# Kernel optimization log

Hardware: AMD Instinct MI355X
Metric: run time of the kernel (lower is better)

## Reference

```python
import jax, jax.numpy as jnp
import numpy as np

B, T, D, CHUNK = 8, 4096, 256, 64
ETA_SCALE = 1e-3
EPS = 1e-6


def setup_inputs() -> dict:
    key = jax.random.key(0)
    ks = jax.random.split(key, 16)
    s = 1.0 / np.sqrt(D)
    def w(k, shape):
        return jax.random.uniform(k, shape, jnp.float32, -s, s)
    return {
        'x': jax.random.normal(ks[0], (B, T, D), jnp.float32),
        'k_w1': w(ks[1], (D, D)), 'k_w2': w(ks[2], (D, D)),
        'v_w1': w(ks[3], (D, D)), 'v_w2': w(ks[4], (D, D)),
        'q_w1': w(ks[5], (D, D)), 'q_w2': w(ks[6], (D, D)),
        'eta_w1': w(ks[7], (1, D)), 'eta_w2': w(ks[8], (D, D)), 'eta_wskip': w(ks[9], (1, D)),
        'alpha_w1': w(ks[10], (1, D)), 'alpha_w2': w(ks[11], (D, D)), 'alpha_wskip': w(ks[12], (1, D)),
        'mem_w1': w(ks[13], (D, D)), 'mem_w2': w(ks[14], (D, D)),
    }


def _gelu(z):
    return jax.nn.gelu(z, approximate=False)  # torch F.gelu default = exact erf gelu


def _dgelu(z):
    # d/dz [z * Phi(z)] = Phi(z) + z * pdf(z)
    cdf = 0.5 * (1.0 + jax.lax.erf(z * (1.0 / np.sqrt(2.0))))
    pdf = jnp.exp(-0.5 * z * z) * (1.0 / np.sqrt(2.0 * np.pi))
    return cdf + z * pdf


def _mem_fwd(x, w1, w2, wskip):
    z = jnp.einsum('bti,bhi->bth', x, w2)
    h = _gelu(z)
    res = x if wskip is None else jnp.einsum('bti,boi->bto', x, wskip)
    return res + jnp.einsum('bth,boh->bto', h, w1)


def _l2norm(q):
    n = jnp.sqrt(jnp.sum(q * q, axis=-1, keepdims=True))
    return q / jnp.maximum(n, EPS)


def _update(st, k, v, eta, abar):
    # chunked DGD: theta <- (prod_t alpha_t) * theta - sum_t eta_t * grad ||M(k_t) - v_t||^2
    w1, w2, wskip = st
    z = jnp.einsum('bti,bhi->bth', k, w2)
    h = _gelu(z)
    res = k if wskip is None else jnp.einsum('bti,boi->bto', k, wskip)
    f = res + jnp.einsum('bth,boh->bto', h, w1)  # [b,t,out]
    if w1.shape[1] == v.shape[-1]:
        g = 2.0 * (f - v)
    else:  # out_dim==1 memories: broadcasted l2 -> reduce over broadcast dim
        g = 2.0 * jnp.sum(f - v, axis=-1, keepdims=True)
    gW1 = jnp.einsum('bto,bth,bt->boh', g, h, eta)
    pre = jnp.einsum('bto,boh->bth', g, w1) * _dgelu(z)
    gW2 = jnp.einsum('bth,bti,bt->bhi', pre, k, eta)
    a = abar[:, None, None]
    nskip = None if wskip is None else a * wskip - jnp.einsum('bto,bti,bt->boi', g, k, eta)
    return (a * w1 - gW1, a * w2 - gW2, nskip)


def _forward(x, k_w1, k_w2, v_w1, v_w2, q_w1, q_w2, eta_w1, eta_w2, eta_wskip,
             alpha_w1, alpha_w2, alpha_wskip, mem_w1, mem_w2):
    b, t, d = x.shape
    def bt(w):
        return jnp.broadcast_to(w[None], (b,) + w.shape)
    states = (
        (bt(k_w1), bt(k_w2), None),
        (bt(v_w1), bt(v_w2), None),
        (bt(q_w1), bt(q_w2), None),
        (bt(eta_w1), bt(eta_w2), bt(eta_wskip)),
        (bt(alpha_w1), bt(alpha_w2), bt(alpha_wskip)),
        (bt(mem_w1), bt(mem_w2), None),
    )
    nc = t // CHUNK
    xc = x.reshape(b, nc, CHUNK, d).transpose(1, 0, 2, 3)  # [NC, B, C, D]

    def step(states, xch):
        sk, sv, sq, se, sa, sm = states
        k = _l2norm(_mem_fwd(xch, *sk))
        v = _mem_fwd(xch, *sv)
        q = _l2norm(_mem_fwd(xch, *sq))
        eta = jax.nn.softplus(_mem_fwd(xch, *se)[..., 0]) * ETA_SCALE
        alpha = jax.nn.sigmoid(_mem_fwd(xch, *sa)[..., 0])
        o = _mem_fwd(q, *sm)
        abar = jnp.prod(alpha, axis=1)  # [b]
        new = tuple(_update(s, k, v, eta, abar) for s in (sk, sv, sq, se, sa, sm))
        return new, o

    _, ys = jax.lax.scan(step, states, xc)  # [NC, B, C, D]
    return ys.transpose(1, 0, 2, 3).reshape(b, t, d)


def reference(x, k_w1, k_w2, v_w1, v_w2, q_w1, q_w2, eta_w1, eta_w2, eta_wskip,
              alpha_w1, alpha_w2, alpha_wskip, mem_w1, mem_w2):
    return _forward(x, k_w1, k_w2, v_w1, v_w2, q_w1, q_w2, eta_w1, eta_w2, eta_wskip,
                    alpha_w1, alpha_w2, alpha_wskip, mem_w1, mem_w2)
```

## Files before the change

### kernel.cpp

```cpp
#include <hip/hip_runtime.h>
#include <hip/hip_bf16.h>
#include <math.h>

constexpr int NB  = 8;
constexpr int TT  = 4096;
constexpr int DD  = 256;
constexpr int CK  = 64;
constexpr int NCK = 64;
constexpr float ETA_SC = 1e-3f;
constexpr float EPSV   = 1e-6f;

constexpr size_t MSZ = (size_t)DD*DD;

constexpr size_t OFF_W2  = 0;
constexpr size_t OFF_W1B = OFF_W2  + (size_t)NB*6*MSZ;
constexpr size_t OFF_W1S = OFF_W1B + (size_t)NB*4*MSZ;
constexpr size_t OFF_WSK = OFF_W1S + (size_t)NB*2*DD;
constexpr size_t OFF_SCK = OFF_WSK + (size_t)NB*2*DD;
constexpr size_t OFF_SCQ = OFF_SCK + (size_t)NB*CK;
constexpr size_t OFF_VSUM= OFF_SCQ + (size_t)NB*CK;
constexpr size_t OFF_ETA = OFF_VSUM+ (size_t)NB*CK;
constexpr size_t OFF_GS  = OFF_ETA + (size_t)NB*CK;
constexpr size_t OFF_SALP= OFF_GS  + (size_t)NB*2*CK;
constexpr size_t OFF_ABAR= OFF_SALP+ (size_t)NB*CK;
constexpr size_t OFF_BARC= OFF_ABAR + NB;
constexpr size_t FTOT    = OFF_BARC + NB;

constexpr size_t BOFF_F  = 0;
constexpr size_t BOFF_H  = BOFF_F  + (size_t)3*NB*CK*DD;
constexpr size_t BOFF_GB = BOFF_H  + (size_t)NB*6*CK*DD;
constexpr size_t BOFF_P  = BOFF_GB + (size_t)NB*4*CK*DD;

__device__ __forceinline__ int bigIdx(int m){ return (m==5)?3:m; }

__device__ __forceinline__ float geluf(float z){
  return 0.5f*z*(1.0f + erff(z*0.70710678118654752440f));
}
__device__ __forceinline__ float dgeluf(float z){
  float cdf = 0.5f*(1.0f + erff(z*0.70710678118654752440f));
  float pdf = expf(-0.5f*z*z)*0.39894228040143267794f;
  return cdf + z*pdf;
}
__device__ __forceinline__ float bfu(unsigned short u){
  unsigned int v = ((unsigned int)u)<<16;
  return __uint_as_float(v);
}
__device__ __forceinline__ float wsum(float v){
  #pragma unroll
  for (int off=32; off>0; off>>=1) v += __shfl_xor(v, off, 64);
  return v;
}

__device__ __forceinline__ void bbar(unsigned int* cnt, unsigned int target){
  __syncthreads();
  if (threadIdx.x == 0){
    __threadfence();
    atomicAdd(cnt, 1u);
    unsigned int it = 0;
    while (__hip_atomic_load(cnt, __ATOMIC_RELAXED, __HIP_MEMORY_SCOPE_AGENT) < target
           && ++it < (1u<<18))
      __builtin_amdgcn_s_sleep(2);
    __threadfence();
  }
  __syncthreads();
}

__device__ __forceinline__ void gfull(const float* __restrict__ sA,
      const float* __restrict__ Wm, int cg, int rg, float acc[4][4]){
  #pragma unroll 4
  for (int kk=0; kk<256; kk+=4){
    float4 w0 = *(const float4*)(Wm + (size_t)(cg      )*DD + kk);
    float4 w1 = *(const float4*)(Wm + (size_t)(cg +  64)*DD + kk);
    float4 w2 = *(const float4*)(Wm + (size_t)(cg + 128)*DD + kk);
    float4 w3 = *(const float4*)(Wm + (size_t)(cg + 192)*DD + kk);
    #pragma unroll
    for (int rr=0; rr<4; rr++){
      float4 a = *(const float4*)(sA + (rg*4+rr)*260 + kk);
      acc[rr][0] += a.x*w0.x + a.y*w0.y + a.z*w0.z + a.w*w0.w;
      acc[rr][1] += a.x*w1.x + a.y*w1.y + a.z*w1.z + a.w*w1.w;
      acc[rr][2] += a.x*w2.x + a.y*w2.y + a.z*w2.z + a.w*w2.w;
      acc[rr][3] += a.x*w3.x + a.y*w3.y + a.z*w3.z + a.w*w3.w;
    }
  }
}

__device__ __forceinline__ void gfullT(const float* __restrict__ sA,
      const float* __restrict__ Wm, int cg, int rg, float acc[4][4]){
  #pragma unroll 2
  for (int kk=0; kk<256; kk+=4){
    float wv[4][4];
    #pragma unroll
    for (int s=0;s<4;s++)
      #pragma unroll
      for (int j=0;j<4;j++)
        wv[s][j] = Wm[(size_t)(kk+s)*DD + cg+64*j];
    #pragma unroll
    for (int rr=0;rr<4;rr++){
      float4 a = *(const float4*)(sA + (rg*4+rr)*260 + kk);
      #pragma unroll
      for (int j=0;j<4;j++)
        acc[rr][j] += a.x*wv[0][j] + a.y*wv[1][j] + a.z*wv[2][j] + a.w*wv[3][j];
    }
  }
}

__global__ __launch_bounds__(256) void initk(float* __restrict__ W,
  const float* kw1, const float* kw2, const float* vw1, const float* vw2,
  const float* qw1, const float* qw2, const float* ew1, const float* ew2,
  const float* ewsk, const float* aw1, const float* aw2, const float* awsk,
  const float* mw1, const float* mw2)
{
  int b = blockIdx.x/6, m = blockIdx.x%6;
  const float *w1s=nullptr,*w2s=nullptr,*wsks=nullptr;
  switch(m){
    case 0: w1s=kw1; w2s=kw2; break;
    case 1: w1s=vw1; w2s=vw2; break;
    case 2: w1s=qw1; w2s=qw2; break;
    case 3: w1s=ew1; w2s=ew2; wsks=ewsk; break;
    case 4: w1s=aw1; w2s=aw2; wsks=awsk; break;
    default: w1s=mw1; w2s=mw2; break;
  }
  if (m==0 && threadIdx.x==0)
    ((unsigned int*)(W + OFF_BARC))[b] = 0u;
  float* w2d = W + OFF_W2 + ((size_t)b*6+m)*MSZ;
  for (size_t i=threadIdx.x; i<MSZ; i+=256) w2d[i] = w2s[i];
  if (m==3 || m==4){
    int sm = m-3;
    float* w1d = W + OFF_W1S + ((size_t)b*2+sm)*DD;
    float* wsd = W + OFF_WSK + ((size_t)b*2+sm)*DD;
    for (int i=threadIdx.x;i<DD;i+=256){ w1d[i]=w1s[i]; wsd[i]=wsks[i]; }
  } else {
    float* w1d = W + OFF_W1B + ((size_t)b*4+bigIdx(m))*MSZ;
    for (size_t i=threadIdx.x;i<MSZ;i+=256) w1d[i] = w1s[i];
  }
}

__global__ __launch_bounds__(256, 1) void pers(const float* __restrict__ x,
        float* __restrict__ W, __hip_bfloat16* __restrict__ B,
        float* __restrict__ out)
{
  const int blk = blockIdx.x, tid = threadIdx.x;
  const int b = blk & 7, wb = blk >> 3;
  const int cg = tid & 63, rg = tid >> 6;
  unsigned int* cnt = ((unsigned int*)(W + OFF_BARC)) + b;
  unsigned int bar = 0;
  __shared__ __align__(16) float sMem[2*16*260];
  __shared__ float sSc[64];
  __shared__ float sEt[64], sSk[64];
  float* sX = sMem;
  float* sY = sMem + 16*260;

  for (int ck=0; ck<NCK; ck++){
    for (int task=wb; task<20; task+=32){
      int m = task>>2, t0 = (task&3)*16;
      const float* xp = x + ((size_t)b*TT + (size_t)ck*CK + t0)*DD;
      for (int l=tid; l<1024; l+=256){
        int tl = l>>6, ii = (l&63)<<2;
        *(float4*)(sX + tl*260 + ii) = *(const float4*)(xp + (size_t)tl*DD + ii);
      }
      __syncthreads();
      const float* w2 = W + OFF_W2 + ((size_t)b*6+m)*MSZ;
      float acc1[4][4];
      #pragma unroll
      for (int i=0;i<4;i++){ acc1[i][0]=acc1[i][1]=acc1[i][2]=acc1[i][3]=0.0f; }
      gfull(sX, w2, cg, rg, acc1);
      if (m < 3){
        #pragma unroll
        for (int rr=0;rr<4;rr++)
          #pragma unroll
          for (int j=0;j<4;j++)
            sY[(rg*4+rr)*260 + cg+64*j] = geluf(acc1[rr][j]);
        __syncthreads();
        const float* w1 = W + OFF_W1B + ((size_t)b*4+m)*MSZ;
        float acc2[4][4];
        #pragma unroll
        for (int i=0;i<4;i++){ acc2[i][0]=acc2[i][1]=acc2[i][2]=acc2[i][3]=0.0f; }
        gfull(sY, w1, cg, rg, acc2);
        __hip_bfloat16* fd = B + BOFF_F + ((size_t)m*NB + b)*CK*DD;
        float p[4];
        #pragma unroll
        for (int rr=0;rr<4;rr++){
          float ps = 0.0f;
          #pragma unroll
          for (int j=0;j<4;j++){
            int col = cg+64*j;
            float F = sX[(rg*4+rr)*260 + col] + acc2[rr][j];
            fd[(size_t)(t0+rg*4+rr)*DD + col] = __float2bfloat16(F);
            ps += (m==1) ? F : F*F;
          }
          p[rr] = ps;
        }
        #pragma unroll
        for (int rr=0;rr<4;rr++){
          float v = wsum(p[rr]);
          if (cg == 0){
            int t = t0 + rg*4 + rr;
            if (m==0)      W[OFF_SCK + (size_t)b*CK + t] = 1.0f/fmaxf(sqrtf(v), EPSV);
            else if (m==2) W[OFF_SCQ + (size_t)b*CK + t] = 1.0f/fmaxf(sqrtf(v), EPSV);
            else           W[OFF_VSUM+ (size_t)b*CK + t] = v;
          }
        }
      } else {
        int sm = m-3;
        const float* w1s = W + OFF_W1S + ((size_t)b*2+sm)*DD;
        const float* wsk = W + OFF_WSK + ((size_t)b*2+sm)*DD;
        float p[4];
        #pragma unroll
        for (int rr=0;rr<4;rr++){
          float ps = 0.0f;
          #pragma unroll
          for (int j=0;j<4;j++){
            int col = cg+64*j;
            ps += sX[(rg*4+rr)*260+col]*wsk[col] + geluf(acc1[rr][j])*w1s[col];
          }
          p[rr] = ps;
        }
        #pragma unroll
        for (int rr=0;rr<4;rr++){
          float v = wsum(p[rr]);
          if (cg == 0){
            int t = t0 + rg*4 + rr;
            if (sm==0){
              float sp = (v>0.0f) ? (v + log1pf(expf(-v))) : log1pf(expf(v));
              W[OFF_ETA + (size_t)b*CK + t] = sp*ETA_SC;
            } else {
              W[OFF_SALP + (size_t)b*CK + t] = 1.0f/(1.0f+expf(-v));
            }
          }
        }
      }
      __syncthreads();
    }
    bar += 32; bbar(cnt, bar);

    for (int task=wb; task<29; task+=32){
      if (task < 28){
        int chn = task>>2, t0 = (task&3)*16;
        bool isq = (chn==6);
        const unsigned short* fsrc = (const unsigned short*)
            (B + BOFF_F + ((size_t)(isq?2:0)*NB + b)*CK*DD + (size_t)t0*DD);
        const float* scp = W + (isq?OFF_SCQ:OFF_SCK) + (size_t)b*CK + t0;
        if (tid < 16)       sSc[tid] = scp[tid];
        else if (tid < 32)  sSc[tid] = W[OFF_ETA + (size_t)b*CK + t0 + (tid-16)];
        else if (tid < 48)  sSc[tid] = W[OFF_VSUM+ (size_t)b*CK + t0 + (tid-32)];
        __syncthreads();
        for (int l=tid; l<1024; l+=256){
          int tl = l>>6, ii = (l&63)<<2;
          ushort4 u = *(const ushort4*)(fsrc + (size_t)tl*DD + ii);
          float s = sSc[tl];
          float4 t4;
          t4.x = bfu(u.x)*s; t4.y = bfu(u.y)*s; t4.z = bfu(u.z)*s; t4.w = bfu(u.w)*s;
          *(float4*)(sX + tl*260 + ii) = t4;
        }
        __syncthreads();
        int m2 = isq ? 5 : chn;
        const float* w2 = W + OFF_W2 + ((size_t)b*6+m2)*MSZ;
        float acc1[4][4];
        #pragma unroll
        for (int i=0;i<4;i++){ acc1[i][0]=acc1[i][1]=acc1[i][2]=acc1[i][3]=0.0f; }
        gfull(sX, w2, cg, rg, acc1);

        if (chn==0 || chn==1 || chn==2 || chn==5){
          int mi = (chn==5)?3:chn;
          __hip_bfloat16* hd = B + BOFF_H + ((size_t)(b*6+chn))*CK*DD;
          #pragma unroll
          for (int rr=0;rr<4;rr++)
            #pragma unroll
            for (int j=0;j<4;j++){
              float h = geluf(acc1[rr][j]);
              sY[(rg*4+rr)*260 + cg+64*j] = h;
              hd[(size_t)(t0+rg*4+rr)*DD + cg+64*j] = __float2bfloat16(h);
            }
          __syncthreads();
          const float* w1 = W + OFF_W1B + ((size_t)b*4+mi)*MSZ;
          float acc2[4][4];
          #pragma unroll
          for (int i=0;i<4;i++){ acc2[i][0]=acc2[i][1]=acc2[i][2]=acc2[i][3]=0.0f; }
          gfull(sY, w1, cg, rg, acc2);
          __syncthreads();
          const unsigned short* fv = (const unsigned short*)
              (B + BOFF_F + ((size_t)1*NB + b)*CK*DD + (size_t)t0*DD);
          __hip_bfloat16* gd = B + BOFF_GB + ((size_t)(b*4+mi))*CK*DD;
          #pragma unroll
          for (int rr=0;rr<4;rr++)
            #pragma unroll
            for (int j=0;j<4;j++){
              int col = cg+64*j;
              float g = 2.0f*( sX[(rg*4+rr)*260+col] + acc2[rr][j]
                               - bfu(fv[(size_t)(rg*4+rr)*DD+col]) );
              sY[(rg*4+rr)*260+col] = g;
              gd[(size_t)(t0+rg*4+rr)*DD + col] = __float2bfloat16(g);
            }
          __syncthreads();
          float accp[4][4];
          #pragma unroll
          for (int i=0;i<4;i++){ accp[i][0]=accp[i][1]=accp[i][2]=accp[i][3]=0.0f; }
          gfullT(sY, w1, cg, rg, accp);
          __hip_bfloat16* pd2 = B + BOFF_P + ((size_t)(b*6+chn))*CK*DD;
          #pragma unroll
          for (int rr=0;rr<4;rr++){
            float et = sSc[16 + rg*4+rr];
            #pragma unroll
            for (int j=0;j<4;j++)
              pd2[(size_t)(t0+rg*4+rr)*DD + cg+64*j] =
                __float2bfloat16(accp[rr][j]*dgeluf(acc1[rr][j])*et);
          }
        } else if (chn==6){
          #pragma unroll
          for (int rr=0;rr<4;rr++)
            #pragma unroll
            for (int j=0;j<4;j++)
              sY[(rg*4+rr)*260 + cg+64*j] = geluf(acc1[rr][j]);
          __syncthreads();
          const float* w1 = W + OFF_W1B + ((size_t)b*4+3)*MSZ;
          float acc2[4][4];
          #pragma unroll
          for (int i=0;i<4;i++){ acc2[i][0]=acc2[i][1]=acc2[i][2]=acc2[i][3]=0.0f; }
          gfull(sY, w1, cg, rg, acc2);
          float* op = out + ((size_t)b*TT + (size_t)ck*CK + t0)*DD;
          #pragma unroll
          for (int rr=0;rr<4;rr++)
            #pragma unroll
            for (int j=0;j<4;j++){
              int col = cg+64*j;
              op[(size_t)(rg*4+rr)*DD + col] = sX[(rg*4+rr)*260+col] + acc2[rr][j];
            }
        } else {
          int sm = chn-3;
          __hip_bfloat16* hd = B + BOFF_H + ((size_t)(b*6+chn))*CK*DD;
          const float* w1s = W + OFF_W1S + ((size_t)b*2+sm)*DD;
          const float* wsk = W + OFF_WSK + ((size_t)b*2+sm)*DD;
          float p[4];
          #pragma unroll
          for (int rr=0;rr<4;rr++){
            float ps = 0.0f;
            #pragma unroll
            for (int j=0;j<4;j++){
              int col = cg+64*j;
              float h = geluf(acc1[rr][j]);
              hd[(size_t)(t0+rg*4+rr)*DD + col] = __float2bfloat16(h);
              ps += sX[(rg*4+rr)*260+col]*wsk[col] + h*w1s[col];
            }
            p[rr] = ps;
          }
          __hip_bfloat16* pd2 = B + BOFF_P + ((size_t)(b*6+chn))*CK*DD;
          #pragma unroll
          for (int rr=0;rr<4;rr++){
            float f = wsum(p[rr]);
            int t = t0 + rg*4 + rr;
            float gs = 2.0f*(256.0f*f - sSc[32 + rg*4+rr]);
            if (cg == 0) W[OFF_GS + ((size_t)b*2+sm)*CK + t] = gs;
            float ge = gs * sSc[16 + rg*4+rr];
            #pragma unroll
            for (int j=0;j<4;j++){
              int col = cg+64*j;
              pd2[(size_t)t*DD + col] =
                __float2bfloat16(ge*w1s[col]*dgeluf(acc1[rr][j]));
            }
          }
        }
      } else {
        if (tid < 64){
          float v = W[OFF_SALP + (size_t)b*CK + tid];
          #pragma unroll
          for (int off=32; off>0; off>>=1) v *= __shfl_xor(v, off, 64);
          if (tid == 0) W[OFF_ABAR + b] = v;
        }
      }
      __syncthreads();
    }
    bar += 32; bbar(cnt, bar);

    {
      if (tid < 64){
        sEt[tid] = W[OFF_ETA + (size_t)b*CK + tid];
        sSk[tid] = W[OFF_SCK + (size_t)b*CK + tid];
      }
      __syncthreads();
      float ab = W[OFF_ABAR + b];
      const unsigned short* fk = (const unsigned short*)(B + BOFF_F + ((size_t)0*NB+b)*CK*DD);
      float* sT = sMem;
      int c = tid;
      for (int task=wb; task<82; task+=32){
        if (task < 32){
          int mi = task>>3, o0 = (task&7)*32;
          int m = (mi==3)?5:mi;
          const unsigned short* hb = (const unsigned short*)(B + BOFF_H + ((size_t)(b*6+m))*CK*DD);
          const unsigned short* gb = (const unsigned short*)(B + BOFF_GB + ((size_t)(b*4+mi))*CK*DD);
          float* w1 = W + OFF_W1B + ((size_t)b*4+mi)*MSZ;
          float hv[64];
          #pragma unroll
          for (int t=0;t<64;t++) hv[t] = bfu(hb[(size_t)t*DD + c]);
          for (int l=tid; l<2048; l+=256){
            int t=l>>5, oo=l&31;
            sT[oo*68+t] = bfu(gb[(size_t)t*DD + o0+oo]) * sEt[t];
          }
          __syncthreads();
          for (int oo=0; oo<32; oo++){
            float s = 0.0f;
            #pragma unroll
            for (int t4=0; t4<16; t4++){
              float4 g4 = *(const float4*)(sT + oo*68 + t4*4);
              s += g4.x*hv[4*t4] + g4.y*hv[4*t4+1] + g4.z*hv[4*t4+2] + g4.w*hv[4*t4+3];
            }
            size_t idx = (size_t)(o0+oo)*DD + c;
            w1[idx] = ab*w1[idx] - s;
          }
        } else if (task < 80){
          int r = task-32, m = r>>3, h0 = (r&7)*32;
          const unsigned short* pd2 = (const unsigned short*)(B + BOFF_P + ((size_t)(b*6+m))*CK*DD);
          float* w2 = W + OFF_W2 + ((size_t)b*6+m)*MSZ;
          float kc[64];
          #pragma unroll
          for (int t=0;t<64;t++) kc[t] = bfu(fk[(size_t)t*DD+c]) * sSk[t];
          for (int l=tid; l<2048; l+=256){
            int t=l>>5, hh=l&31;
            sT[hh*68+t] = bfu(pd2[(size_t)t*DD + h0+hh]);
          }
          __syncthreads();
          for (int hh=0; hh<32; hh++){
            float s = 0.0f;
            #pragma unroll
            for (int t4=0; t4<16; t4++){
              float4 p4 = *(const float4*)(sT + hh*68 + t4*4);
              s += p4.x*kc[4*t4] + p4.y*kc[4*t4+1] + p4.z*kc[4*t4+2] + p4.w*kc[4*t4+3];
            }
            size_t idx = (size_t)(h0+hh)*DD + c;
            w2[idx] = ab*w2[idx] - s;
          }
        } else {
          int sm = task-80, m = 3+sm;
          const unsigned short* hb = (const unsigned short*)(B + BOFF_H + ((size_t)(b*6+m))*CK*DD);
          float s1=0.0f, s2=0.0f;
          #pragma unroll
          for (int t=0;t<64;t++){
            float ge = W[OFF_GS + ((size_t)b*2+sm)*CK + t] * sEt[t];
            s1 += ge * bfu(hb[(size_t)t*DD+c]);
            s2 += ge * bfu(fk[(size_t)t*DD+c]) * sSk[t];
          }
          float* w1s = W + OFF_W1S + ((size_t)b*2+sm)*DD;
          float* wskp= W + OFF_WSK + ((size_t)b*2+sm)*DD;
          w1s[c]  = ab*w1s[c]  - s1;
          wskp[c] = ab*wskp[c] - s2;
        }
        __syncthreads();
      }
    }
    bar += 32; bbar(cnt, bar);
  }
}

extern "C" void kernel_launch(void* const* d_in, const int* in_sizes, int n_in,
                              void* d_out, int out_size, void* d_ws, size_t ws_size,
                              hipStream_t stream){
  const float* x = (const float*)d_in[0];
  float* W = (float*)d_ws;
  __hip_bfloat16* B = (__hip_bfloat16*)(W + FTOT);
  float* out = (float*)d_out;

  initk<<<NB*6, 256, 0, stream>>>(W,
      (const float*)d_in[1], (const float*)d_in[2],
      (const float*)d_in[3], (const float*)d_in[4],
      (const float*)d_in[5], (const float*)d_in[6],
      (const float*)d_in[7], (const float*)d_in[8],
      (const float*)d_in[9], (const float*)d_in[10],
      (const float*)d_in[11], (const float*)d_in[12],
      (const float*)d_in[13], (const float*)d_in[14]);

  pers<<<256, 256, 0, stream>>>(x, W, B, out);
}
```

Baseline: 15.06 ms.

## Store weights transposed for coalesced GEMV loads and keep dual W1 copies

Weights are now stored transposed (W2T, W1T) so each thread reads contiguous float4 columns, which coalesces the global loads in the forward GEMMs. A second, untransposed W1 copy serves the backward product, replacing the strided gfullT path. Stores of h, g and p switch to vectorized ushort4 and float4, and the update phase is retiled into 64-wide tasks. The cost is updating two copies of W1 per chunk, extra memory, and fewer update tasks, so load balance across the 32 worker blocks changes.

```diff
diff --git a/kernel.cpp b/kernel.cpp
--- a/kernel.cpp
+++ b/kernel.cpp
@@ -12,9 +12,10 @@
 
 constexpr size_t MSZ = (size_t)DD*DD;
 
-constexpr size_t OFF_W2  = 0;
-constexpr size_t OFF_W1B = OFF_W2  + (size_t)NB*6*MSZ;
-constexpr size_t OFF_W1S = OFF_W1B + (size_t)NB*4*MSZ;
+constexpr size_t OFF_W2T = 0;
+constexpr size_t OFF_W1T = OFF_W2T + (size_t)NB*6*MSZ;
+constexpr size_t OFF_W1N = OFF_W1T + (size_t)NB*4*MSZ;
+constexpr size_t OFF_W1S = OFF_W1N + (size_t)NB*4*MSZ;
 constexpr size_t OFF_WSK = OFF_W1S + (size_t)NB*2*DD;
 constexpr size_t OFF_SCK = OFF_WSK + (size_t)NB*2*DD;
 constexpr size_t OFF_SCQ = OFF_SCK + (size_t)NB*CK;
@@ -45,6 +46,10 @@
   unsigned int v = ((unsigned int)u)<<16;
   return __uint_as_float(v);
 }
+__device__ __forceinline__ unsigned short f2bu(float f){
+  __hip_bfloat16 h = __float2bfloat16(f);
+  union { __hip_bfloat16 b; unsigned short u; } cv; cv.b = h; return cv.u;
+}
 __device__ __forceinline__ float wsum(float v){
   #pragma unroll
   for (int off=32; off>0; off>>=1) v += __shfl_xor(v, off, 64);
@@ -65,41 +70,22 @@
   __syncthreads();
 }
 
-__device__ __forceinline__ void gfull(const float* __restrict__ sA,
-      const float* __restrict__ Wm, int cg, int rg, float acc[4][4]){
+__device__ __forceinline__ void gcoal(const float* __restrict__ sA,
+      const float* __restrict__ Mt, int cg, int rg, float acc[4][4]){
+  const float* mp = Mt + 4*cg;
   #pragma unroll 4
   for (int kk=0; kk<256; kk+=4){
-    float4 w0 = *(const float4*)(Wm + (size_t)(cg      )*DD + kk);
-    float4 w1 = *(const float4*)(Wm + (size_t)(cg +  64)*DD + kk);
-    float4 w2 = *(const float4*)(Wm + (size_t)(cg + 128)*DD + kk);
-    float4 w3 = *(const float4*)(Wm + (size_t)(cg + 192)*DD + kk);
+    float4 w0 = *(const float4*)(mp + (size_t)(kk  )*DD);
+    float4 w1 = *(const float4*)(mp + (size_t)(kk+1)*DD);
+    float4 w2 = *(const float4*)(mp + (size_t)(kk+2)*DD);
+    float4 w3 = *(const float4*)(mp + (size_t)(kk+3)*DD);
     #pragma unroll
     for (int rr=0; rr<4; rr++){
       float4 a = *(const float4*)(sA + (rg*4+rr)*260 + kk);
-      acc[rr][0] += a.x*w0.x + a.y*w0.y + a.z*w0.z + a.w*w0.w;
-      acc[rr][1] += a.x*w1.x + a.y*w1.y + a.z*w1.z + a.w*w1.w;
-      acc[rr][2] += a.x*w2.x + a.y*w2.y + a.z*w2.z + a.w*w2.w;
-      acc[rr][3] += a.x*w3.x + a.y*w3.y + a.z*w3.z + a.w*w3.w;
-    }
-  }
-}
-
-__device__ __forceinline__ void gfullT(const float* __restrict__ sA,
-      const float* __restrict__ Wm, int cg, int rg, float acc[4][4]){
-  #pragma unroll 2
-  for (int kk=0; kk<256; kk+=4){
-    float wv[4][4];
-    #pragma unroll
-    for (int s=0;s<4;s++)
-      #pragma unroll
-      for (int j=0;j<4;j++)
-        wv[s][j] = Wm[(size_t)(kk+s)*DD + cg+64*j];
-    #pragma unroll
-    for (int rr=0;rr<4;rr++){
-      float4 a = *(const float4*)(sA + (rg*4+rr)*260 + kk);
-      #pragma unroll
-      for (int j=0;j<4;j++)
-        acc[rr][j] += a.x*wv[0][j] + a.y*wv[1][j] + a.z*wv[2][j] + a.w*wv[3][j];
+      acc[rr][0] += a.x*w0.x + a.y*w1.x + a.z*w2.x + a.w*w3.x;
+      acc[rr][1] += a.x*w0.y + a.y*w1.y + a.z*w2.y + a.w*w3.y;
+      acc[rr][2] += a.x*w0.z + a.y*w1.z + a.z*w2.z + a.w*w3.z;
+      acc[rr][3] += a.x*w0.w + a.y*w1.w + a.z*w2.w + a.w*w3.w;
     }
   }
 }
@@ -111,34 +97,44 @@
   const float* mw1, const float* mw2)
 {
   int b = blockIdx.x/6, m = blockIdx.x%6;
-  const float *w1s=nullptr,*w2s=nullptr,*wsks=nullptr;
+  const float *w1src=nullptr,*w2src=nullptr,*wsks=nullptr;
   switch(m){
-    case 0: w1s=kw1; w2s=kw2; break;
-    case 1: w1s=vw1; w2s=vw2; break;
-    case 2: w1s=qw1; w2s=qw2; break;
-    case 3: w1s=ew1; w2s=ew2; wsks=ewsk; break;
-    case 4: w1s=aw1; w2s=aw2; wsks=awsk; break;
-    default: w1s=mw1; w2s=mw2; break;
+    case 0: w1src=kw1; w2src=kw2; break;
+    case 1: w1src=vw1; w2src=vw2; break;
+    case 2: w1src=qw1; w2src=qw2; break;
+    case 3: w1src=ew1; w2src=ew2; wsks=ewsk; break;
+    case 4: w1src=aw1; w2src=aw2; wsks=awsk; break;
+    default: w1src=mw1; w2src=mw2; break;
   }
   if (m==0 && threadIdx.x==0)
     ((unsigned int*)(W + OFF_BARC))[b] = 0u;
-  float* w2d = W + OFF_W2 + ((size_t)b*6+m)*MSZ;
-  for (size_t i=threadIdx.x; i<MSZ; i+=256) w2d[i] = w2s[i];
+  float* w2t = W + OFF_W2T + ((size_t)b*6+m)*MSZ;
+  for (size_t l=threadIdx.x; l<MSZ; l+=256){
+    size_t i = l>>8, h = l&255;
+    w2t[l] = w2src[h*(size_t)DD + i];
+  }
   if (m==3 || m==4){
     int sm = m-3;
     float* w1d = W + OFF_W1S + ((size_t)b*2+sm)*DD;
     float* wsd = W + OFF_WSK + ((size_t)b*2+sm)*DD;
-    for (int i=threadIdx.x;i<DD;i+=256){ w1d[i]=w1s[i]; wsd[i]=wsks[i]; }
+    for (int i=threadIdx.x;i<DD;i+=256){ w1d[i]=w1src[i]; wsd[i]=wsks[i]; }
   } else {
-    float* w1d = W + OFF_W1B + ((size_t)b*4+bigIdx(m))*MSZ;
-    for (size_t i=threadIdx.x;i<MSZ;i+=256) w1d[i] = w1s[i];
+    int mi = bigIdx(m);
+    float* w1t = W + OFF_W1T + ((size_t)b*4+mi)*MSZ;
+    float* w1n = W + OFF_W1N + ((size_t)b*4+mi)*MSZ;
+    for (size_t l=threadIdx.x; l<MSZ; l+=256){
+      size_t h = l>>8, o = l&255;
+      w1t[l] = w1src[o*(size_t)DD + h];
+      w1n[l] = w1src[l];
+    }
   }
 }
 
 __global__ __launch_bounds__(256, 1) void pers(const float* __restrict__ x,
-        float* __restrict__ W, __hip_bfloat16* __restrict__ B,
+        float* __restrict__ W, __hip_bfloat16* __restrict__ Bb,
         float* __restrict__ out)
 {
+  unsigned short* B = (unsigned short*)Bb;
   const int blk = blockIdx.x, tid = threadIdx.x;
   const int b = blk & 7, wb = blk >> 3;
   const int cg = tid & 63, rg = tid >> 6;
@@ -159,36 +155,33 @@
         *(float4*)(sX + tl*260 + ii) = *(const float4*)(xp + (size_t)tl*DD + ii);
       }
       __syncthreads();
-      const float* w2 = W + OFF_W2 + ((size_t)b*6+m)*MSZ;
       float acc1[4][4];
       #pragma unroll
       for (int i=0;i<4;i++){ acc1[i][0]=acc1[i][1]=acc1[i][2]=acc1[i][3]=0.0f; }
-      gfull(sX, w2, cg, rg, acc1);
+      gcoal(sX, W + OFF_W2T + ((size_t)b*6+m)*MSZ, cg, rg, acc1);
       if (m < 3){
         #pragma unroll
-        for (int rr=0;rr<4;rr++)
-          #pragma unroll
-          for (int j=0;j<4;j++)
-            sY[(rg*4+rr)*260 + cg+64*j] = geluf(acc1[rr][j]);
+        for (int rr=0;rr<4;rr++){
+          float4 h4;
+          h4.x=geluf(acc1[rr][0]); h4.y=geluf(acc1[rr][1]);
+          h4.z=geluf(acc1[rr][2]); h4.w=geluf(acc1[rr][3]);
+          *(float4*)(sY + (rg*4+rr)*260 + 4*cg) = h4;
+        }
         __syncthreads();
-        const float* w1 = W + OFF_W1B + ((size_t)b*4+m)*MSZ;
         float acc2[4][4];
         #pragma unroll
         for (int i=0;i<4;i++){ acc2[i][0]=acc2[i][1]=acc2[i][2]=acc2[i][3]=0.0f; }
-        gfull(sY, w1, cg, rg, acc2);
-        __hip_bfloat16* fd = B + BOFF_F + ((size_t)m*NB + b)*CK*DD;
+        gcoal(sY, W + OFF_W1T + ((size_t)b*4+m)*MSZ, cg, rg, acc2);
+        unsigned short* fd = B + BOFF_F + ((size_t)m*NB + b)*CK*DD;
         float p[4];
         #pragma unroll
         for (int rr=0;rr<4;rr++){
-          float ps = 0.0f;
-          #pragma unroll
-          for (int j=0;j<4;j++){
-            int col = cg+64*j;
-            float F = sX[(rg*4+rr)*260 + col] + acc2[rr][j];
-            fd[(size_t)(t0+rg*4+rr)*DD + col] = __float2bfloat16(F);
-            ps += (m==1) ? F : F*F;
-          }
-          p[rr] = ps;
+          float4 xv = *(const float4*)(sX + (rg*4+rr)*260 + 4*cg);
+          float F0=xv.x+acc2[rr][0], F1=xv.y+acc2[rr][1];
+          float F2=xv.z+acc2[rr][2], F3=xv.w+acc2[rr][3];
+          ushort4 u; u.x=f2bu(F0); u.y=f2bu(F1); u.z=f2bu(F2); u.w=f2bu(F3);
+          *(ushort4*)(fd + (size_t)(t0+rg*4+rr)*DD + 4*cg) = u;
+          p[rr] = (m==1) ? (F0+F1+F2+F3) : (F0*F0+F1*F1+F2*F2+F3*F3);
         }
         #pragma unroll
         for (int rr=0;rr<4;rr++){
@@ -204,16 +197,15 @@
         int sm = m-3;
         const float* w1s = W + OFF_W1S + ((size_t)b*2+sm)*DD;
         const float* wsk = W + OFF_WSK + ((size_t)b*2+sm)*DD;
+        float4 w1v = *(const float4*)(w1s + 4*cg);
+        float4 wkv = *(const float4*)(wsk + 4*cg);
         float p[4];
         #pragma unroll
         for (int rr=0;rr<4;rr++){
-          float ps = 0.0f;
-          #pragma unroll
-          for (int j=0;j<4;j++){
-            int col = cg+64*j;
-            ps += sX[(rg*4+rr)*260+col]*wsk[col] + geluf(acc1[rr][j])*w1s[col];
-          }
-          p[rr] = ps;
+          float4 xv = *(const float4*)(sX + (rg*4+rr)*260 + 4*cg);
+          p[rr] = xv.x*wkv.x + xv.y*wkv.y + xv.z*wkv.z + xv.w*wkv.w
+                + geluf(acc1[rr][0])*w1v.x + geluf(acc1[rr][1])*w1v.y
+                + geluf(acc1[rr][2])*w1v.z + geluf(acc1[rr][3])*w1v.w;
         }
         #pragma unroll
         for (int rr=0;rr<4;rr++){
@@ -237,8 +229,8 @@
       if (task < 28){
         int chn = task>>2, t0 = (task&3)*16;
         bool isq = (chn==6);
-        const unsigned short* fsrc = (const unsigned short*)
-            (B + BOFF_F + ((size_t)(isq?2:0)*NB + b)*CK*DD + (size_t)t0*DD);
+        const unsigned short* fsrc = B + BOFF_F + ((size_t)(isq?2:0)*NB + b)*CK*DD
+                                       + (size_t)t0*DD;
         const float* scp = W + (isq?OFF_SCQ:OFF_SCK) + (size_t)b*CK + t0;
         if (tid < 16)       sSc[tid] = scp[tid];
         else if (tid < 32)  sSc[tid] = W[OFF_ETA + (size_t)b*CK + t0 + (tid-16)];
@@ -254,96 +246,102 @@
         }
         __syncthreads();
         int m2 = isq ? 5 : chn;
-        const float* w2 = W + OFF_W2 + ((size_t)b*6+m2)*MSZ;
         float acc1[4][4];
         #pragma unroll
         for (int i=0;i<4;i++){ acc1[i][0]=acc1[i][1]=acc1[i][2]=acc1[i][3]=0.0f; }
-        gfull(sX, w2, cg, rg, acc1);
+        gcoal(sX, W + OFF_W2T + ((size_t)b*6+m2)*MSZ, cg, rg, acc1);
 
         if (chn==0 || chn==1 || chn==2 || chn==5){
           int mi = (chn==5)?3:chn;
-          __hip_bfloat16* hd = B + BOFF_H + ((size_t)(b*6+chn))*CK*DD;
-          #pragma unroll
-          for (int rr=0;rr<4;rr++)
-            #pragma unroll
-            for (int j=0;j<4;j++){
-              float h = geluf(acc1[rr][j]);
-              sY[(rg*4+rr)*260 + cg+64*j] = h;
-              hd[(size_t)(t0+rg*4+rr)*DD + cg+64*j] = __float2bfloat16(h);
-            }
-          __syncthreads();
-          const float* w1 = W + OFF_W1B + ((size_t)b*4+mi)*MSZ;
+          unsigned short* hd = B + BOFF_H + ((size_t)(b*6+chn))*CK*DD;
+          #pragma unroll
+          for (int rr=0;rr<4;rr++){
+            float4 h4;
+            h4.x=geluf(acc1[rr][0]); h4.y=geluf(acc1[rr][1]);
+            h4.z=geluf(acc1[rr][2]); h4.w=geluf(acc1[rr][3]);
+            *(float4*)(sY + (rg*4+rr)*260 + 4*cg) = h4;
+            ushort4 hu; hu.x=f2bu(h4.x); hu.y=f2bu(h4.y); hu.z=f2bu(h4.z); hu.w=f2bu(h4.w);
+            *(ushort4*)(hd + (size_t)(t0+rg*4+rr)*DD + 4*cg) = hu;
+          }
+          __syncthreads();
           float acc2[4][4];
           #pragma unroll
           for (int i=0;i<4;i++){ acc2[i][0]=acc2[i][1]=acc2[i][2]=acc2[i][3]=0.0f; }
-          gfull(sY, w1, cg, rg, acc2);
-          __syncthreads();
-          const unsigned short* fv = (const unsigned short*)
-              (B + BOFF_F + ((size_t)1*NB + b)*CK*DD + (size_t)t0*DD);
-          __hip_bfloat16* gd = B + BOFF_GB + ((size_t)(b*4+mi))*CK*DD;
-          #pragma unroll
-          for (int rr=0;rr<4;rr++)
-            #pragma unroll
-            for (int j=0;j<4;j++){
-              int col = cg+64*j;
-              float g = 2.0f*( sX[(rg*4+rr)*260+col] + acc2[rr][j]
-                               - bfu(fv[(size_t)(rg*4+rr)*DD+col]) );
-              sY[(rg*4+rr)*260+col] = g;
-              gd[(size_t)(t0+rg*4+rr)*DD + col] = __float2bfloat16(g);
-            }
+          gcoal(sY, W + OFF_W1T + ((size_t)b*4+mi)*MSZ, cg, rg, acc2);
+          __syncthreads();
+          const unsigned short* fvp = B + BOFF_F + ((size_t)1*NB + b)*CK*DD
+                                        + (size_t)t0*DD;
+          unsigned short* gd = B + BOFF_GB + ((size_t)(b*4+mi))*CK*DD;
+          #pragma unroll
+          for (int rr=0;rr<4;rr++){
+            float4 xv = *(const float4*)(sX + (rg*4+rr)*260 + 4*cg);
+            ushort4 fv4 = *(const ushort4*)(fvp + (size_t)(rg*4+rr)*DD + 4*cg);
+            float4 g4;
+            g4.x = 2.0f*(xv.x + acc2[rr][0] - bfu(fv4.x));
+            g4.y = 2.0f*(xv.y + acc2[rr][1] - bfu(fv4.y));
+            g4.z = 2.0f*(xv.z + acc2[rr][2] - bfu(fv4.z));
+            g4.w = 2.0f*(xv.w + acc2[rr][3] - bfu(fv4.w));
+            *(float4*)(sY + (rg*4+rr)*260 + 4*cg) = g4;
+            ushort4 gu; gu.x=f2bu(g4.x); gu.y=f2bu(g4.y); gu.z=f2bu(g4.z); gu.w=f2bu(g4.w);
+            *(ushort4*)(gd + (size_t)(t0+rg*4+rr)*DD + 4*cg) = gu;
+          }
           __syncthreads();
           float accp[4][4];
           #pragma unroll
           for (int i=0;i<4;i++){ accp[i][0]=accp[i][1]=accp[i][2]=accp[i][3]=0.0f; }
-          gfullT(sY, w1, cg, rg, accp);
-          __hip_bfloat16* pd2 = B + BOFF_P + ((size_t)(b*6+chn))*CK*DD;
+          gcoal(sY, W + OFF_W1N + ((size_t)b*4+mi)*MSZ, cg, rg, accp);
+          unsigned short* pd2 = B + BOFF_P + ((size_t)(b*6+chn))*CK*DD;
           #pragma unroll
           for (int rr=0;rr<4;rr++){
             float et = sSc[16 + rg*4+rr];
-            #pragma unroll
-            for (int j=0;j<4;j++)
-              pd2[(size_t)(t0+rg*4+rr)*DD + cg+64*j] =
-                __float2bfloat16(accp[rr][j]*dgeluf(acc1[rr][j])*et);
+            ushort4 pu;
+            pu.x = f2bu(accp[rr][0]*dgeluf(acc1[rr][0])*et);
+            pu.y = f2bu(accp[rr][1]*dgeluf(acc1[rr][1])*et);
+            pu.z = f2bu(accp[rr][2]*dgeluf(acc1[rr][2])*et);
+            pu.w = f2bu(accp[rr][3]*dgeluf(acc1[rr][3])*et);
+            *(ushort4*)(pd2 + (size_t)(t0+rg*4+rr)*DD + 4*cg) = pu;
           }
         } else if (chn==6){
           #pragma unroll
-          for (int rr=0;rr<4;rr++)
-            #pragma unroll
-            for (int j=0;j<4;j++)
-              sY[(rg*4+rr)*260 + cg+64*j] = geluf(acc1[rr][j]);
-          __syncthreads();
-          const float* w1 = W + OFF_W1B + ((size_t)b*4+3)*MSZ;
+          for (int rr=0;rr<4;rr++){
+            float4 h4;
+            h4.x=geluf(acc1[rr][0]); h4.y=geluf(acc1[rr][1]);
+            h4.z=geluf(acc1[rr][2]); h4.w=geluf(acc1[rr][3]);
+            *(float4*)(sY + (rg*4+rr)*260 + 4*cg) = h4;
+          }
+          __syncthreads();
           float acc2[4][4];
           #pragma unroll
           for (int i=0;i<4;i++){ acc2[i][0]=acc2[i][1]=acc2[i][2]=acc2[i][3]=0.0f; }
-          gfull(sY, w1, cg, rg, acc2);
+          gcoal(sY, W + OFF_W1T + ((size_t)b*4+3)*MSZ, cg, rg, acc2);
           float* op = out + ((size_t)b*TT + (size_t)ck*CK + t0)*DD;
           #pragma unroll
-          for (int rr=0;rr<4;rr++)
-            #pragma unroll
-            for (int j=0;j<4;j++){
-              int col = cg+64*j;
-              op[(size_t)(rg*4+rr)*DD + col] = sX[(rg*4+rr)*260+col] + acc2[rr][j];
-            }
+          for (int rr=0;rr<4;rr++){
+            float4 xv = *(const float4*)(sX + (rg*4+rr)*260 + 4*cg);
+            float4 o4;
+            o4.x = xv.x + acc2[rr][0]; o4.y = xv.y + acc2[rr][1];
+            o4.z = xv.z + acc2[rr][2]; o4.w = xv.w + acc2[rr][3];
+            *(float4*)(op + (size_t)(rg*4+rr)*DD + 4*cg) = o4;
+          }
         } else {
           int sm = chn-3;
-          __hip_bfloat16* hd = B + BOFF_H + ((size_t)(b*6+chn))*CK*DD;
+          unsigned short* hd = B + BOFF_H + ((size_t)(b*6+chn))*CK*DD;
           const float* w1s = W + OFF_W1S + ((size_t)b*2+sm)*DD;
           const float* wsk = W + OFF_WSK + ((size_t)b*2+sm)*DD;
+          float4 w1v = *(const float4*)(w1s + 4*cg);
+          float4 wkv = *(const float4*)(wsk + 4*cg);
           float p[4];
           #pragma unroll
           for (int rr=0;rr<4;rr++){
-            float ps = 0.0f;
-            #pragma unroll
-            for (int j=0;j<4;j++){
-              int col = cg+64*j;
-              float h = geluf(acc1[rr][j]);
-              hd[(size_t)(t0+rg*4+rr)*DD + col] = __float2bfloat16(h);
-              ps += sX[(rg*4+rr)*260+col]*wsk[col] + h*w1s[col];
-            }
-            p[rr] = ps;
-          }
-          __hip_bfloat16* pd2 = B + BOFF_P + ((size_t)(b*6+chn))*CK*DD;
+            float4 xv = *(const float4*)(sX + (rg*4+rr)*260 + 4*cg);
+            float h0=geluf(acc1[rr][0]), h1=geluf(acc1[rr][1]);
+            float h2=geluf(acc1[rr][2]), h3=geluf(acc1[rr][3]);
+            ushort4 hu; hu.x=f2bu(h0); hu.y=f2bu(h1); hu.z=f2bu(h2); hu.w=f2bu(h3);
+            *(ushort4*)(hd + (size_t)(t0+rg*4+rr)*DD + 4*cg) = hu;
+            p[rr] = xv.x*wkv.x + xv.y*wkv.y + xv.z*wkv.z + xv.w*wkv.w
+                  + h0*w1v.x + h1*w1v.y + h2*w1v.z + h3*w1v.w;
+          }
+          unsigned short* pd2 = B + BOFF_P + ((size_t)(b*6+chn))*CK*DD;
           #pragma unroll
           for (int rr=0;rr<4;rr++){
             float f = wsum(p[rr]);
@@ -351,12 +349,12 @@
             float gs = 2.0f*(256.0f*f - sSc[32 + rg*4+rr]);
             if (cg == 0) W[OFF_GS + ((size_t)b*2+sm)*CK + t] = gs;
             float ge = gs * sSc[16 + rg*4+rr];
-            #pragma unroll
-            for (int j=0;j<4;j++){
-              int col = cg+64*j;
-              pd2[(size_t)t*DD + col] =
-                __float2bfloat16(ge*w1s[col]*dgeluf(acc1[rr][j]));
-            }
+            ushort4 pu;
+            pu.x = f2bu(ge*w1v.x*dgeluf(acc1[rr][0]));
+            pu.y = f2bu(ge*w1v.y*dgeluf(acc1[rr][1]));
+            pu.z = f2bu(ge*w1v.z*dgeluf(acc1[rr][2]));
+            pu.w = f2bu(ge*w1v.w*dgeluf(acc1[rr][3]));
+            *(ushort4*)(pd2 + (size_t)t*DD + 4*cg) = pu;
           }
         }
       } else {
@@ -378,25 +376,25 @@
       }
       __syncthreads();
       float ab = W[OFF_ABAR + b];
-      const unsigned short* fk = (const unsigned short*)(B + BOFF_F + ((size_t)0*NB+b)*CK*DD);
+      const unsigned short* fk = B + BOFF_F + ((size_t)0*NB+b)*CK*DD;
       float* sT = sMem;
       int c = tid;
-      for (int task=wb; task<82; task+=32){
-        if (task < 32){
-          int mi = task>>3, o0 = (task&7)*32;
+      for (int task=wb; task<58; task+=32){
+        if (task < 16){
+          int mi = task>>2, o0 = (task&3)*64;
           int m = (mi==3)?5:mi;
-          const unsigned short* hb = (const unsigned short*)(B + BOFF_H + ((size_t)(b*6+m))*CK*DD);
-          const unsigned short* gb = (const unsigned short*)(B + BOFF_GB + ((size_t)(b*4+mi))*CK*DD);
-          float* w1 = W + OFF_W1B + ((size_t)b*4+mi)*MSZ;
+          const unsigned short* hb = B + BOFF_H + ((size_t)(b*6+m))*CK*DD;
+          const unsigned short* gb = B + BOFF_GB + ((size_t)(b*4+mi))*CK*DD;
+          float* w1n = W + OFF_W1N + ((size_t)b*4+mi)*MSZ;
           float hv[64];
           #pragma unroll
           for (int t=0;t<64;t++) hv[t] = bfu(hb[(size_t)t*DD + c]);
-          for (int l=tid; l<2048; l+=256){
-            int t=l>>5, oo=l&31;
+          for (int l=tid; l<4096; l+=256){
+            int t=l>>6, oo=l&63;
             sT[oo*68+t] = bfu(gb[(size_t)t*DD + o0+oo]) * sEt[t];
           }
           __syncthreads();
-          for (int oo=0; oo<32; oo++){
+          for (int oo=0; oo<64; oo++){
             float s = 0.0f;
             #pragma unroll
             for (int t4=0; t4<16; t4++){
@@ -404,33 +402,57 @@
               s += g4.x*hv[4*t4] + g4.y*hv[4*t4+1] + g4.z*hv[4*t4+2] + g4.w*hv[4*t4+3];
             }
             size_t idx = (size_t)(o0+oo)*DD + c;
-            w1[idx] = ab*w1[idx] - s;
-          }
-        } else if (task < 80){
-          int r = task-32, m = r>>3, h0 = (r&7)*32;
-          const unsigned short* pd2 = (const unsigned short*)(B + BOFF_P + ((size_t)(b*6+m))*CK*DD);
-          float* w2 = W + OFF_W2 + ((size_t)b*6+m)*MSZ;
-          float kc[64];
-          #pragma unroll
-          for (int t=0;t<64;t++) kc[t] = bfu(fk[(size_t)t*DD+c]) * sSk[t];
-          for (int l=tid; l<2048; l+=256){
-            int t=l>>5, hh=l&31;
-            sT[hh*68+t] = bfu(pd2[(size_t)t*DD + h0+hh]);
-          }
-          __syncthreads();
-          for (int hh=0; hh<32; hh++){
+            w1n[idx] = ab*w1n[idx] - s;
+          }
+        } else if (task < 32){
+          int r = task-16, mi = r>>2, h0 = (r&3)*64;
+          int m = (mi==3)?5:mi;
+          const unsigned short* hb = B + BOFF_H + ((size_t)(b*6+m))*CK*DD;
+          const unsigned short* gb = B + BOFF_GB + ((size_t)(b*4+mi))*CK*DD;
+          float* w1t = W + OFF_W1T + ((size_t)b*4+mi)*MSZ;
+          float gv[64];
+          #pragma unroll
+          for (int t=0;t<64;t++) gv[t] = bfu(gb[(size_t)t*DD + c]) * sEt[t];
+          for (int l=tid; l<4096; l+=256){
+            int t=l>>6, hh=l&63;
+            sT[hh*68+t] = bfu(hb[(size_t)t*DD + h0+hh]);
+          }
+          __syncthreads();
+          for (int hh=0; hh<64; hh++){
             float s = 0.0f;
             #pragma unroll
             for (int t4=0; t4<16; t4++){
-              float4 p4 = *(const float4*)(sT + hh*68 + t4*4);
-              s += p4.x*kc[4*t4] + p4.y*kc[4*t4+1] + p4.z*kc[4*t4+2] + p4.w*kc[4*t4+3];
+              float4 h4 = *(const float4*)(sT + hh*68 + t4*4);
+              s += h4.x*gv[4*t4] + h4.y*gv[4*t4+1] + h4.z*gv[4*t4+2] + h4.w*gv[4*t4+3];
             }
             size_t idx = (size_t)(h0+hh)*DD + c;
-            w2[idx] = ab*w2[idx] - s;
+            w1t[idx] = ab*w1t[idx] - s;
+          }
+        } else if (task < 56){
+          int r = task-32, m = r>>2, i0 = (r&3)*64;
+          const unsigned short* pd = B + BOFF_P + ((size_t)(b*6+m))*CK*DD;
+          float* w2t = W + OFF_W2T + ((size_t)b*6+m)*MSZ;
+          float pv[64];
+          #pragma unroll
+          for (int t=0;t<64;t++) pv[t] = bfu(pd[(size_t)t*DD + c]);
+          for (int l=tid; l<4096; l+=256){
+            int t=l>>6, ii=l&63;
+            sT[ii*68+t] = bfu(fk[(size_t)t*DD + i0+ii]) * sSk[t];
+          }
+          __syncthreads();
+          for (int ii=0; ii<64; ii++){
+            float s = 0.0f;
+            #pragma unroll
+            for (int t4=0; t4<16; t4++){
+              float4 k4 = *(const float4*)(sT + ii*68 + t4*4);
+              s += k4.x*pv[4*t4] + k4.y*pv[4*t4+1] + k4.z*pv[4*t4+2] + k4.w*pv[4*t4+3];
+            }
+            size_t idx = (size_t)(i0+ii)*DD + c;
+            w2t[idx] = ab*w2t[idx] - s;
           }
         } else {
-          int sm = task-80, m = 3+sm;
-          const unsigned short* hb = (const unsigned short*)(B + BOFF_H + ((size_t)(b*6+m))*CK*DD);
+          int sm = task-56, m = 3+sm;
+          const unsigned short* hb = B + BOFF_H + ((size_t)(b*6+m))*CK*DD;
           float s1=0.0f, s2=0.0f;
           #pragma unroll
           for (int t=0;t<64;t++){
```

After: 13.26 ms. 12.0% less time.
